# Optimization experiments

Measured on AMD Instinct MI355X. Metric: run time of the kernel, lower is better.

## Reference

```python
import jax, jax.numpy as jnp
import numpy as np

B, T, H, L, V = 32, 512, 1024, 256, 13  # V = FDIM_JOINT_VOCAB_DECODING


def setup_inputs() -> dict:
    key = jax.random.key(0)
    ks = jax.random.split(key, 16)
    s_in = 1.0 / np.sqrt(V)
    s_h = 1.0 / np.sqrt(H)
    s_l = 1.0 / np.sqrt(L)
    s_hl = 1.0 / np.sqrt(H + L)
    # one-hot-like teacher-forced inputs (first token is all-zero start token)
    labels = jax.random.randint(ks[0], (B, T), 0, V)
    seq_input = jax.nn.one_hot(labels, V, dtype=jnp.float32)
    seq_input = jnp.concatenate([jnp.zeros((B, 1, V), jnp.float32), seq_input[:, :-1]], axis=1)
    lengths = jax.random.randint(ks[1], (B,), T // 2, T + 1).astype(jnp.int32)
    return {
        "seq_input": seq_input,
        "latent_vec": jax.random.normal(ks[2], (B, L), jnp.float32),
        "labels": labels.astype(jnp.int32),
        "lengths": lengths,
        "W_ih": jax.random.uniform(ks[3], (4 * H, V), jnp.float32, -s_h, s_h),
        "W_hh": jax.random.uniform(ks[4], (4 * H, H), jnp.float32, -s_h, s_h),
        "b_ih": jax.random.uniform(ks[5], (4 * H,), jnp.float32, -s_h, s_h),
        "b_hh": jax.random.uniform(ks[6], (4 * H,), jnp.float32, -s_h, s_h),
        "Wz": jax.random.uniform(ks[7], (H, L), jnp.float32, -s_l, s_l),
        "bz": jax.random.uniform(ks[8], (H,), jnp.float32, -s_l, s_l),
        "Wnl": jax.random.uniform(ks[9], (H, H + L), jnp.float32, -s_hl, s_hl),
        "bnl": jax.random.uniform(ks[10], (H,), jnp.float32, -s_hl, s_hl),
        "Wout": jax.random.uniform(ks[11], (V, H), jnp.float32, -s_h, s_h),
        "bout": jax.random.uniform(ks[12], (V,), jnp.float32, -s_h, s_h),
    }


def _forward(seq_input, latent_vec, labels, lengths,
             W_ih, W_hh, b_ih, b_hh, Wz, bz, Wnl, bnl, Wout, bout):
    h0 = jax.nn.relu(latent_vec @ Wz.T + bz)              # [B,H]
    c0 = jnp.zeros_like(h0)

    def step(carry, x_t):
        h, c = carry
        gates = x_t @ W_ih.T + b_ih + h @ W_hh.T + b_hh   # [B,4H]
        i, f, g, o = jnp.split(gates, 4, axis=-1)         # torch LSTMCell gate order
        c = jax.nn.sigmoid(f) * c + jax.nn.sigmoid(i) * jnp.tanh(g)
        h = jax.nn.sigmoid(o) * jnp.tanh(c)
        return (h, c), h

    xs = jnp.swapaxes(seq_input, 0, 1)                    # [T,B,V]
    _, hs = jax.lax.scan(step, (h0, c0), xs)              # [T,B,H]
    hs = jnp.swapaxes(hs, 0, 1)                           # [B,T,H]

    # aggregate: cat(h, z) -> relu(W_nonlinear) -> W
    lat = jnp.broadcast_to(latent_vec[:, None, :], (hs.shape[0], hs.shape[1], latent_vec.shape[-1]))
    feat = jnp.concatenate([hs, lat], axis=-1)            # [B,T,H+L]
    logits = jax.nn.relu(feat @ Wnl.T + bnl) @ Wout.T + bout  # [B,T,V]

    logp = jax.nn.log_softmax(logits, axis=-1)
    nll = -jnp.take_along_axis(logp, labels[..., None].astype(jnp.int32), axis=-1)[..., 0]  # [B,T]
    mask = (jnp.arange(T)[None, :] < lengths[:, None]).astype(nll.dtype)
    batch_loss = jnp.sum(nll * mask, axis=1)              # per-sequence segment sum
    return batch_loss


def reference(seq_input, latent_vec, labels, lengths,
              W_ih, W_hh, b_ih, b_hh, Wz, bz, Wnl, bnl, Wout, bout):
    batch_loss = _forward(seq_input, latent_vec, labels, lengths,
                          W_ih, W_hh, b_ih, b_hh, Wz, bz, Wnl, bnl, Wout, bout)
    return jnp.sum(batch_loss), batch_loss
```

## Files before the change

### kernel.cpp

```cpp
#include <hip/hip_runtime.h>
#include <hip/hip_bf16.h>

#define B_   32
#define T_   512
#define H_   1024
#define L_   256
#define V_   13
#define G4H  4096
#define KHL  1280

typedef float f32x4 __attribute__((ext_vector_type(4)));
typedef short s16x8 __attribute__((ext_vector_type(8)));
typedef unsigned short u16;
typedef unsigned int   u32;
typedef unsigned long long u64;

#define OFF_BF   33619968u
#define OFF_BF2  42008576u
#define OFF_AZ   44630016u
#define OFF_BAR  44646400u
#define OFF_MID  44650496u
#define OFF_GX   OFF_MID
#define OFF_TOK  (OFF_MID + 229376u)

__device__ __forceinline__ u16 f2bf(float f) {
    union { float f; u32 u; } v; v.f = f;
    u32 u = v.u;
    u32 r = (u + 0x7fffu + ((u >> 16) & 1u)) >> 16;
    return (u16)r;
}
__device__ __forceinline__ float bf2f(u16 h) {
    union { u32 u; float f; } v; v.u = ((u32)h) << 16;
    return v.f;
}
__device__ __forceinline__ float sigm_(float x) {
    x = fminf(fmaxf(x, -30.f), 30.f);
    return 1.f / (1.f + __expf(-x));
}
__device__ __forceinline__ float tanh_(float x) {
    x = fminf(fmaxf(x, -15.f), 15.f);
    float e = __expf(2.f * x);
    return (e - 1.f) / (e + 1.f);
}

__device__ __forceinline__ u32 afrag_pos(int bl, int k) {
    return (u32)((k >> 5) * 512 + ((bl | (((k >> 3) & 3) << 4)) << 3) + (k & 7));
}

__global__ __launch_bounds__(256) void k_init_misc(
        const float* __restrict__ latent, const float* __restrict__ Wz,
        const float* __restrict__ bz,
        u16* __restrict__ Ax, u16* __restrict__ Az, int* __restrict__ bar) {
    int gid = blockIdx.x * 256 + threadIdx.x;
    int b = gid >> 10, j = gid & 1023;
    const float* lrow = latent + b * L_;
    const float* wrow = Wz + j * L_;
    float acc = bz[j];
    #pragma unroll 4
    for (int l = 0; l < L_; ++l) acc += lrow[l] * wrow[l];
    Ax[(b >> 4) * 16384 + afrag_pos(b & 15, j)] = f2bf(fmaxf(acc, 0.f));
    if (gid < B_ * L_) {
        int bb = gid >> 8, l = gid & 255;
        Az[(bb >> 4) * 4096 + afrag_pos(bb & 15, l)] = f2bf(latent[gid]);
    }
    if (gid < 1024) bar[gid] = 0;
}

__global__ __launch_bounds__(256) void k_init_gx(
        const float* __restrict__ W_ih, const float* __restrict__ b_ih,
        const float* __restrict__ b_hh, float* __restrict__ Gx) {
    int row = blockIdx.x * 256 + threadIdx.x;
    if (row >= G4H) return;
    int gg = row >> 10, jg = row & 1023;
    float base = b_ih[row] + b_hh[row];
    float* d = Gx + (size_t)jg * 56;
    const float* wr = W_ih + (size_t)row * V_;
    #pragma unroll
    for (int t = 0; t < V_; ++t) d[t * 4 + gg] = base + wr[t];
    d[13 * 4 + gg] = base;
}

__global__ __launch_bounds__(256) void k_init_tok(
        const float* __restrict__ seq, u16* __restrict__ tok) {
    int gid = blockIdx.x * 256 + threadIdx.x;
    int s = gid >> 5, b = gid & 31;
    const float* r = seq + ((size_t)b * T_ + s) * V_;
    int t = 13;
    #pragma unroll
    for (int v = 0; v < V_; ++v) if (r[v] > 0.5f) t = v;
    tok[gid] = (u16)t;
}

__global__ __launch_bounds__(256) void k_init_wfrag(
        const float* __restrict__ W_hh, u16* __restrict__ Bf) {
    int base = blockIdx.x * 256 + threadIdx.x;
    #pragma unroll
    for (int i = 0; i < 8; ++i) {
        int idx = base + i * 524288;
        int jv   = idx & 7;
        int lane = (idx >> 3) & 63;
        int kc   = (idx >> 9) & 31;
        int nt   = idx >> 14;
        int u = lane & 15;
        int row = (u & 3) * H_ + nt * 4 + (u >> 2);
        int k = kc * 32 + (lane >> 4) * 8 + jv;
        Bf[idx] = f2bf(W_hh[row * H_ + k]);
    }
}

__global__ __launch_bounds__(256) void k_init_wfrag2(
        const float* __restrict__ Wnl, u16* __restrict__ Bf2) {
    int idx = blockIdx.x * 256 + threadIdx.x;
    for (; idx < 1310720; idx += 524288) {
        int jv   = idx & 7;
        int lane = (idx >> 3) & 63;
        int q    = idx >> 9;
        int kc   = q % 40;
        int nt2  = q / 40;
        int n = nt2 * 16 + (lane & 15);
        int k = kc * 32 + (lane >> 4) * 8 + jv;
        Bf2[idx] = f2bf(Wnl[n * KHL + k]);
    }
}

__global__ __launch_bounds__(512, 1) void k_recur(
        const u16* __restrict__ tokbuf, const float* __restrict__ Gx,
        const u16* __restrict__ Bf, u16* __restrict__ Ax,
        int* __restrict__ bar) {
    __shared__ uint4 AhV[2048];
    __shared__ int sh_info;
    int tid = threadIdx.x;

    if (tid == 0) {
        u32 xcc = 0;
        asm volatile("s_getreg_b32 %0, hwreg(HW_REG_XCC_ID)" : "=s"(xcc));
        xcc &= 7u;
        int t = -1;
        if (xcc < 2u) {
            int tk = __hip_atomic_fetch_add(bar + (int)xcc * 512, 1,
                         __ATOMIC_RELAXED, __HIP_MEMORY_SCOPE_AGENT);
            if (tk < 32) t = ((int)xcc << 5) | tk;
        }
        sh_info = t;
    }
    __syncthreads();
    int info = sh_info;
    if (info < 0) return;
    int mt = info >> 5;
    int p  = info & 31;

    int w = tid >> 6, L = tid & 63;
    int nt = p * 8 + w;
    int lm = L & 15, quad = L >> 4;

    s16x8 afr[32];
    {
        const u16* bfp = Bf + (size_t)nt * 16384 + L * 8;
        #pragma unroll
        for (int kc = 0; kc < 32; ++kc)
            afr[kc] = *reinterpret_cast<const s16x8*>(bfp + kc * 512);
    }
    int jg = nt * 4 + quad;
    int b = mt * 16 + lm;
    const float* gxp = Gx + (size_t)jg * 56;
    u32 posu16 = (u32)((nt >> 3) * 512 + ((lm | (((nt >> 1) & 3) << 4)) << 3)
                       + (nt & 1) * 4 + quad);
    int* flags = bar + mt * 512 + 16;
    const int* myflag = flags + (w + 8 * (L & 3)) * 8;
    u32* AxD = (u32*)Ax;
    float c = 0.f;

    for (int s = 0; s < T_; ++s) {
        int tok = tokbuf[s * 32 + b];
        float4 gx4 = *reinterpret_cast<const float4*>(gxp + tok * 4);

        for (;;) {
            int v = __hip_atomic_load(myflag, __ATOMIC_RELAXED,
                                      __HIP_MEMORY_SCOPE_AGENT);
            if (__all(v >= s)) break;
            __builtin_amdgcn_s_sleep(1);
        }
        const uint4* srcq = (const uint4*)((const char*)Ax
                             + ((size_t)s * 2 + mt) * 32768);
        #pragma unroll
        for (int i = 0; i < 4; ++i)
            AhV[i * 512 + tid] = srcq[i * 512 + tid];
        __syncthreads();

        f32x4 a0 = {0.f,0.f,0.f,0.f}, a1 = {0.f,0.f,0.f,0.f};
        f32x4 a2 = {0.f,0.f,0.f,0.f}, a3 = {0.f,0.f,0.f,0.f};
        const u16* hp = (const u16*)AhV + L * 8;
        #pragma unroll
        for (int kc = 0; kc < 32; kc += 4) {
            s16x8 h0 = *reinterpret_cast<const s16x8*>(hp + kc * 512);
            s16x8 h1 = *reinterpret_cast<const s16x8*>(hp + (kc + 1) * 512);
            s16x8 h2 = *reinterpret_cast<const s16x8*>(hp + (kc + 2) * 512);
            s16x8 h3 = *reinterpret_cast<const s16x8*>(hp + (kc + 3) * 512);
            a0 = __builtin_amdgcn_mfma_f32_16x16x32_bf16(afr[kc],     h0, a0, 0, 0, 0);
            a1 = __builtin_amdgcn_mfma_f32_16x16x32_bf16(afr[kc + 1], h1, a1, 0, 0, 0);
            a2 = __builtin_amdgcn_mfma_f32_16x16x32_bf16(afr[kc + 2], h2, a2, 0, 0, 0);
            a3 = __builtin_amdgcn_mfma_f32_16x16x32_bf16(afr[kc + 3], h3, a3, 0, 0, 0);
        }
        float gi = a0[0] + a1[0] + a2[0] + a3[0] + gx4.x;
        float gf = a0[1] + a1[1] + a2[1] + a3[1] + gx4.y;
        float gg = a0[2] + a1[2] + a2[2] + a3[2] + gx4.z;
        float go = a0[3] + a1[3] + a2[3] + a3[3] + gx4.w;
        float ig = sigm_(gi), fg = sigm_(gf);
        float gt = tanh_(gg), og = sigm_(go);
        c = fg * c + ig * gt;
        float hv = og * tanh_(c);

        u32 bits = (u32)f2bf(hv);
        u32 other = (u32)(u16)__shfl_xor((int)bits, 16);
        if (!(quad & 1)) {
            u32 word = bits | (other << 16);
            AxD[((size_t)(s + 1) * 2 + mt) * 8192 + (posu16 >> 1)] = word;
        }
        if (s == T_ - 1) break;
        __syncthreads();
        if (tid == 0)
            __hip_atomic_store(flags + p * 8, s + 1, __ATOMIC_RELAXED,
                               __HIP_MEMORY_SCOPE_WORKGROUP);
    }
}

__global__ __launch_bounds__(256) void k_gemm1(
        const u16* __restrict__ Ax, const u16* __restrict__ Az,
        const u16* __restrict__ Bf2, const float* __restrict__ bnl,
        u16* __restrict__ mid) {
    int tid = threadIdx.x;
    int nb = blockIdx.x;
    int mb = blockIdx.y;
    int w = tid >> 6, L = tid & 63;
    int lm = L & 15, quad = L >> 4;
    int mti0 = mb * 8 + w * 2;
    const u16* a0p = Ax + ((size_t)mti0 + 2) * 16384 + L * 8;
    const u16* a1p = a0p + 16384;
    const u16* az0 = Az + L * 8;
    const u16* az1 = az0 + 4096;
    const u16* bp = Bf2 + (size_t)(nb * 4) * 40 * 512 + L * 8;

    f32x4 acc[2][4];
    #pragma unroll
    for (int a = 0; a < 2; ++a)
        #pragma unroll
        for (int n = 0; n < 4; ++n) acc[a][n] = (f32x4){0.f, 0.f, 0.f, 0.f};

    #pragma unroll 4
    for (int kc = 0; kc < 32; ++kc) {
        s16x8 a0 = *reinterpret_cast<const s16x8*>(a0p + kc * 512);
        s16x8 a1 = *reinterpret_cast<const s16x8*>(a1p + kc * 512);
        #pragma unroll
        for (int n4 = 0; n4 < 4; ++n4) {
            s16x8 bv = *reinterpret_cast<const s16x8*>(bp + ((size_t)n4 * 40 + kc) * 512);
            acc[0][n4] = __builtin_amdgcn_mfma_f32_16x16x32_bf16(a0, bv, acc[0][n4], 0, 0, 0);
            acc[1][n4] = __builtin_amdgcn_mfma_f32_16x16x32_bf16(a1, bv, acc[1][n4], 0, 0, 0);
        }
    }
    #pragma unroll
    for (int kc2 = 0; kc2 < 8; ++kc2) {
        s16x8 a0 = *reinterpret_cast<const s16x8*>(az0 + kc2 * 512);
        s16x8 a1 = *reinterpret_cast<const s16x8*>(az1 + kc2 * 512);
        #pragma unroll
        for (int n4 = 0; n4 < 4; ++n4) {
            s16x8 bv = *reinterpret_cast<const s16x8*>(bp + ((size_t)n4 * 40 + 32 + kc2) * 512);
            acc[0][n4] = __builtin_amdgcn_mfma_f32_16x16x32_bf16(a0, bv, acc[0][n4], 0, 0, 0);
            acc[1][n4] = __builtin_amdgcn_mfma_f32_16x16x32_bf16(a1, bv, acc[1][n4], 0, 0, 0);
        }
    }
    #pragma unroll
    for (int mt2 = 0; mt2 < 2; ++mt2)
        #pragma unroll
        for (int n4 = 0; n4 < 4; ++n4)
            #pragma unroll
            for (int r = 0; r < 4; ++r) {
                int m = mb * 128 + w * 32 + mt2 * 16 + quad * 4 + r;
                int n = (nb * 4 + n4) * 16 + lm;
                float v = acc[mt2][n4][r] + bnl[n];
                mid[(size_t)m * H_ + n] = f2bf(fmaxf(v, 0.f));
            }
}

__global__ __launch_bounds__(256) void k_loss(
        const u16* __restrict__ mid, const float* __restrict__ Wout,
        const float* __restrict__ bout, const int* __restrict__ labels,
        const int* __restrict__ lengths, float* __restrict__ out) {
    int mrow = blockIdx.x;
    int b = mrow & 31, t = mrow >> 5;
    if (t >= lengths[b]) return;
    int tid = threadIdx.x;
    float p[V_];
    #pragma unroll
    for (int v = 0; v < V_; ++v) p[v] = 0.f;
    uint2 raw = *reinterpret_cast<const uint2*>(mid + (size_t)mrow * H_ + tid * 4);
    const u16* rs = (const u16*)&raw;
    float mv0 = bf2f(rs[0]), mv1 = bf2f(rs[1]), mv2 = bf2f(rs[2]), mv3 = bf2f(rs[3]);
    #pragma unroll
    for (int v = 0; v < V_; ++v) {
        float4 wv = *reinterpret_cast<const float4*>(Wout + v * H_ + tid * 4);
        p[v] = mv0 * wv.x + mv1 * wv.y + mv2 * wv.z + mv3 * wv.w;
    }
    #pragma unroll
    for (int off = 32; off > 0; off >>= 1)
        #pragma unroll
        for (int v = 0; v < V_; ++v) p[v] += __shfl_down(p[v], off);
    __shared__ float red[4][V_];
    int w = tid >> 6, L = tid & 63;
    if (L == 0)
        #pragma unroll
        for (int v = 0; v < V_; ++v) red[w][v] = p[v];
    __syncthreads();
    if (tid == 0) {
        float lg[V_]; float mx = -1e30f;
        #pragma unroll
        for (int v = 0; v < V_; ++v) {
            lg[v] = red[0][v] + red[1][v] + red[2][v] + red[3][v] + bout[v];
            mx = fmaxf(mx, lg[v]);
        }
        float se = 0.f;
        #pragma unroll
        for (int v = 0; v < V_; ++v) se += __expf(lg[v] - mx);
        float lse = mx + logf(se);
        int lab = labels[b * T_ + t];
        atomicAdd(&out[1 + b], lse - lg[lab]);
    }
}

__global__ void k_final(float* __restrict__ out) {
    float s = 0.f;
    for (int b = 0; b < B_; ++b) s += out[1 + b];
    out[0] = s;
}

extern "C" void kernel_launch(void* const* d_in, const int* in_sizes, int n_in,
                              void* d_out, int out_size, void* d_ws, size_t ws_size,
                              hipStream_t stream) {
    const float* seq    = (const float*)d_in[0];
    const float* latent = (const float*)d_in[1];
    const int*   labels = (const int*)d_in[2];
    const int*   lengths= (const int*)d_in[3];
    const float* W_ih   = (const float*)d_in[4];
    const float* W_hh   = (const float*)d_in[5];
    const float* b_ih   = (const float*)d_in[6];
    const float* b_hh   = (const float*)d_in[7];
    const float* Wz     = (const float*)d_in[8];
    const float* bz     = (const float*)d_in[9];
    const float* Wnl    = (const float*)d_in[10];
    const float* bnl    = (const float*)d_in[11];
    const float* Wout   = (const float*)d_in[12];
    const float* bout   = (const float*)d_in[13];

    char* ws = (char*)d_ws;
    u16*   Ax   = (u16*)(ws);
    u16*   Bf   = (u16*)(ws + OFF_BF);
    u16*   Bf2  = (u16*)(ws + OFF_BF2);
    u16*   Az   = (u16*)(ws + OFF_AZ);
    int*   bar  = (int*)(ws + OFF_BAR);
    u16*   mid  = (u16*)(ws + OFF_MID);
    float* Gx   = (float*)(ws + OFF_GX);
    u16*   tok  = (u16*)(ws + OFF_TOK);
    float* out  = (float*)d_out;

    hipMemsetAsync(d_out, 0, 33 * sizeof(float), stream);
    k_init_misc<<<128, 256, 0, stream>>>(latent, Wz, bz, Ax, Az, bar);
    k_init_gx<<<16, 256, 0, stream>>>(W_ih, b_ih, b_hh, Gx);
    k_init_tok<<<64, 256, 0, stream>>>(seq, tok);
    k_init_wfrag<<<2048, 256, 0, stream>>>(W_hh, Bf);
    k_init_wfrag2<<<2048, 256, 0, stream>>>(Wnl, Bf2);
    k_recur<<<512, 512, 0, stream>>>(tok, Gx, Bf, Ax, bar);
    k_gemm1<<<dim3(16, 128), 256, 0, stream>>>(Ax, Az, Bf2, bnl, mid);
    k_loss<<<16384, 256, 0, stream>>>(mid, Wout, bout, labels, lengths, out);
    k_final<<<1, 1, 0, stream>>>(out);
}
```

Measured before the change: 1.194 ms.

## Split recurrent K dimension across waves with LDS reduction in LSTM step

Each wave now handles four gate tiles over one quarter of the hidden K range instead of one tile over the full K. The partial results are reduced through shared memory by the first wave group, which then applies the gate nonlinearities. This reuses each h fragment across four MFMAs and shortens each wave's serial MFMA chain per step. The cost is an extra barrier and LDS round trip every timestep, and only a quarter of the waves take part in the elementwise phase.

```diff
diff --git a/kernel.cpp b/kernel.cpp
--- a/kernel.cpp
+++ b/kernel.cpp
@@ -128,6 +128,7 @@
         const u16* __restrict__ Bf, u16* __restrict__ Ax,
         int* __restrict__ bar) {
     __shared__ uint4 AhV[2048];
+    __shared__ float redbuf[6][1088];
     __shared__ int sh_info;
     int tid = threadIdx.x;
 
@@ -150,29 +151,42 @@
     int p  = info & 31;
 
     int w = tid >> 6, L = tid & 63;
-    int nt = p * 8 + w;
+    int g = w & 1;
+    int q = w >> 1;
     int lm = L & 15, quad = L >> 4;
-
-    s16x8 afr[32];
-    {
-        const u16* bfp = Bf + (size_t)nt * 16384 + L * 8;
-        #pragma unroll
-        for (int kc = 0; kc < 32; ++kc)
-            afr[kc] = *reinterpret_cast<const s16x8*>(bfp + kc * 512);
-    }
-    int jg = nt * 4 + quad;
+    int nt0 = p * 8 + g * 4;
+
+    s16x8 afr[4][8];
+    #pragma unroll
+    for (int j = 0; j < 4; ++j) {
+        const u16* bfp = Bf + (size_t)(nt0 + j) * 16384 + (q * 8) * 512 + L * 8;
+        #pragma unroll
+        for (int kk = 0; kk < 8; ++kk)
+            afr[j][kk] = *reinterpret_cast<const s16x8*>(bfp + kk * 512);
+    }
     int b = mt * 16 + lm;
-    const float* gxp = Gx + (size_t)jg * 56;
-    u32 posu16 = (u32)((nt >> 3) * 512 + ((lm | (((nt >> 1) & 3) << 4)) << 3)
-                       + (nt & 1) * 4 + quad);
+    const float* gxp[4];
+    u32 pos[4];
+    #pragma unroll
+    for (int j = 0; j < 4; ++j) {
+        int ntj = nt0 + j;
+        gxp[j] = Gx + (size_t)(ntj * 4 + quad) * 56;
+        pos[j] = (u32)((ntj >> 3) * 512 + ((lm | (((ntj >> 1) & 3) << 4)) << 3)
+                       + (ntj & 1) * 4 + quad);
+    }
     int* flags = bar + mt * 512 + 16;
     const int* myflag = flags + (w + 8 * (L & 3)) * 8;
     u32* AxD = (u32*)Ax;
-    float c = 0.f;
+    float c0 = 0.f, c1 = 0.f, c2 = 0.f, c3 = 0.f;
 
     for (int s = 0; s < T_; ++s) {
         int tok = tokbuf[s * 32 + b];
-        float4 gx4 = *reinterpret_cast<const float4*>(gxp + tok * 4);
+        float4 gx4[4];
+        if (q == 0) {
+            #pragma unroll
+            for (int j = 0; j < 4; ++j)
+                gx4[j] = *reinterpret_cast<const float4*>(gxp[j] + tok * 4);
+        }
 
         for (;;) {
             int v = __hip_atomic_load(myflag, __ATOMIC_RELAXED,
@@ -187,34 +201,55 @@
             AhV[i * 512 + tid] = srcq[i * 512 + tid];
         __syncthreads();
 
-        f32x4 a0 = {0.f,0.f,0.f,0.f}, a1 = {0.f,0.f,0.f,0.f};
-        f32x4 a2 = {0.f,0.f,0.f,0.f}, a3 = {0.f,0.f,0.f,0.f};
-        const u16* hp = (const u16*)AhV + L * 8;
-        #pragma unroll
-        for (int kc = 0; kc < 32; kc += 4) {
-            s16x8 h0 = *reinterpret_cast<const s16x8*>(hp + kc * 512);
-            s16x8 h1 = *reinterpret_cast<const s16x8*>(hp + (kc + 1) * 512);
-            s16x8 h2 = *reinterpret_cast<const s16x8*>(hp + (kc + 2) * 512);
-            s16x8 h3 = *reinterpret_cast<const s16x8*>(hp + (kc + 3) * 512);
-            a0 = __builtin_amdgcn_mfma_f32_16x16x32_bf16(afr[kc],     h0, a0, 0, 0, 0);
-            a1 = __builtin_amdgcn_mfma_f32_16x16x32_bf16(afr[kc + 1], h1, a1, 0, 0, 0);
-            a2 = __builtin_amdgcn_mfma_f32_16x16x32_bf16(afr[kc + 2], h2, a2, 0, 0, 0);
-            a3 = __builtin_amdgcn_mfma_f32_16x16x32_bf16(afr[kc + 3], h3, a3, 0, 0, 0);
-        }
-        float gi = a0[0] + a1[0] + a2[0] + a3[0] + gx4.x;
-        float gf = a0[1] + a1[1] + a2[1] + a3[1] + gx4.y;
-        float gg = a0[2] + a1[2] + a2[2] + a3[2] + gx4.z;
-        float go = a0[3] + a1[3] + a2[3] + a3[3] + gx4.w;
-        float ig = sigm_(gi), fg = sigm_(gf);
-        float gt = tanh_(gg), og = sigm_(go);
-        c = fg * c + ig * gt;
-        float hv = og * tanh_(c);
-
-        u32 bits = (u32)f2bf(hv);
-        u32 other = (u32)(u16)__shfl_xor((int)bits, 16);
-        if (!(quad & 1)) {
-            u32 word = bits | (other << 16);
-            AxD[((size_t)(s + 1) * 2 + mt) * 8192 + (posu16 >> 1)] = word;
+        f32x4 acc[4];
+        #pragma unroll
+        for (int j = 0; j < 4; ++j) acc[j] = (f32x4){0.f, 0.f, 0.f, 0.f};
+        const u16* hp = (const u16*)AhV + (q * 8) * 512 + L * 8;
+        #pragma unroll
+        for (int kk = 0; kk < 8; ++kk) {
+            s16x8 h = *reinterpret_cast<const s16x8*>(hp + kk * 512);
+            acc[0] = __builtin_amdgcn_mfma_f32_16x16x32_bf16(afr[0][kk], h, acc[0], 0, 0, 0);
+            acc[1] = __builtin_amdgcn_mfma_f32_16x16x32_bf16(afr[1][kk], h, acc[1], 0, 0, 0);
+            acc[2] = __builtin_amdgcn_mfma_f32_16x16x32_bf16(afr[2][kk], h, acc[2], 0, 0, 0);
+            acc[3] = __builtin_amdgcn_mfma_f32_16x16x32_bf16(afr[3][kk], h, acc[3], 0, 0, 0);
+        }
+        if (q > 0) {
+            float* rb = &redbuf[(q - 1) * 2 + g][L * 17];
+            #pragma unroll
+            for (int j = 0; j < 4; ++j)
+                #pragma unroll
+                for (int r = 0; r < 4; ++r) rb[j * 4 + r] = acc[j][r];
+        }
+        __syncthreads();
+
+        if (q == 0) {
+            #pragma unroll
+            for (int qq = 0; qq < 3; ++qq) {
+                const float* rb = &redbuf[qq * 2 + g][L * 17];
+                #pragma unroll
+                for (int j = 0; j < 4; ++j)
+                    #pragma unroll
+                    for (int r = 0; r < 4; ++r) acc[j][r] += rb[j * 4 + r];
+            }
+            float* cs[4] = {&c0, &c1, &c2, &c3};
+            #pragma unroll
+            for (int j = 0; j < 4; ++j) {
+                float gi = acc[j][0] + gx4[j].x;
+                float gf = acc[j][1] + gx4[j].y;
+                float gg = acc[j][2] + gx4[j].z;
+                float go = acc[j][3] + gx4[j].w;
+                float ig = sigm_(gi), fg = sigm_(gf);
+                float gt = tanh_(gg), og = sigm_(go);
+                float cn = fg * (*cs[j]) + ig * gt;
+                *cs[j] = cn;
+                float hv = og * tanh_(cn);
+                u32 bits = (u32)f2bf(hv);
+                u32 other = (u32)(u16)__shfl_xor((int)bits, 16);
+                if (!(quad & 1)) {
+                    u32 word = bits | (other << 16);
+                    AxD[((size_t)(s + 1) * 2 + mt) * 8192 + (pos[j] >> 1)] = word;
+                }
+            }
         }
         if (s == T_ - 1) break;
         __syncthreads();
```

Result: slower. 1.578 ms (+32.2%).

## Halve recurrent workgroup size, each wave computes two gate tiles

Applied to the files above, without the earlier changes.

The persistent LSTM recurrence kernel now runs 4 waves per block instead of 8, and each wave holds W_hh fragments for two N-tiles (64 VGPR vectors) and reuses every LDS h fragment across both tiles. The h-state copy into LDS and the flag polling pattern are adjusted to match. The aim is to cut per-step LDS reads and barrier cost by sharing loaded h data across two MFMA chains. In exchange, register pressure doubles, which risks spills, and each wave does twice the serial MFMA work per step.

```diff
diff --git a/kernel.cpp b/kernel.cpp
--- a/kernel.cpp
+++ b/kernel.cpp
@@ -123,7 +123,7 @@
     }
 }
 
-__global__ __launch_bounds__(512, 1) void k_recur(
+__global__ __launch_bounds__(256, 1) void k_recur(
         const u16* __restrict__ tokbuf, const float* __restrict__ Gx,
         const u16* __restrict__ Bf, u16* __restrict__ Ax,
         int* __restrict__ bar) {
@@ -150,29 +150,36 @@
     int p  = info & 31;
 
     int w = tid >> 6, L = tid & 63;
-    int nt = p * 8 + w;
     int lm = L & 15, quad = L >> 4;
-
-    s16x8 afr[32];
-    {
-        const u16* bfp = Bf + (size_t)nt * 16384 + L * 8;
+    int nt0 = p * 8 + w * 2;
+
+    s16x8 afr[2][32];
+    #pragma unroll
+    for (int j = 0; j < 2; ++j) {
+        const u16* bfp = Bf + (size_t)(nt0 + j) * 16384 + L * 8;
         #pragma unroll
         for (int kc = 0; kc < 32; ++kc)
-            afr[kc] = *reinterpret_cast<const s16x8*>(bfp + kc * 512);
-    }
-    int jg = nt * 4 + quad;
+            afr[j][kc] = *reinterpret_cast<const s16x8*>(bfp + kc * 512);
+    }
     int b = mt * 16 + lm;
-    const float* gxp = Gx + (size_t)jg * 56;
-    u32 posu16 = (u32)((nt >> 3) * 512 + ((lm | (((nt >> 1) & 3) << 4)) << 3)
-                       + (nt & 1) * 4 + quad);
+    const float* gxp[2];
+    u32 pos[2];
+    #pragma unroll
+    for (int j = 0; j < 2; ++j) {
+        int ntj = nt0 + j;
+        gxp[j] = Gx + (size_t)(ntj * 4 + quad) * 56;
+        pos[j] = (u32)((ntj >> 3) * 512 + ((lm | (((ntj >> 1) & 3) << 4)) << 3)
+                       + (ntj & 1) * 4 + quad);
+    }
     int* flags = bar + mt * 512 + 16;
-    const int* myflag = flags + (w + 8 * (L & 3)) * 8;
+    const int* myflag = flags + (4 * (L & 7) + w) * 8;
     u32* AxD = (u32*)Ax;
-    float c = 0.f;
+    float c0 = 0.f, c1 = 0.f;
 
     for (int s = 0; s < T_; ++s) {
         int tok = tokbuf[s * 32 + b];
-        float4 gx4 = *reinterpret_cast<const float4*>(gxp + tok * 4);
+        float4 gx40 = *reinterpret_cast<const float4*>(gxp[0] + tok * 4);
+        float4 gx41 = *reinterpret_cast<const float4*>(gxp[1] + tok * 4);
 
         for (;;) {
             int v = __hip_atomic_load(myflag, __ATOMIC_RELAXED,
@@ -183,38 +190,50 @@
         const uint4* srcq = (const uint4*)((const char*)Ax
                              + ((size_t)s * 2 + mt) * 32768);
         #pragma unroll
-        for (int i = 0; i < 4; ++i)
-            AhV[i * 512 + tid] = srcq[i * 512 + tid];
+        for (int i = 0; i < 8; ++i)
+            AhV[i * 256 + tid] = srcq[i * 256 + tid];
         __syncthreads();
 
-        f32x4 a0 = {0.f,0.f,0.f,0.f}, a1 = {0.f,0.f,0.f,0.f};
-        f32x4 a2 = {0.f,0.f,0.f,0.f}, a3 = {0.f,0.f,0.f,0.f};
+        f32x4 a00 = {0.f,0.f,0.f,0.f}, a01 = {0.f,0.f,0.f,0.f};
+        f32x4 a10 = {0.f,0.f,0.f,0.f}, a11 = {0.f,0.f,0.f,0.f};
         const u16* hp = (const u16*)AhV + L * 8;
         #pragma unroll
-        for (int kc = 0; kc < 32; kc += 4) {
-            s16x8 h0 = *reinterpret_cast<const s16x8*>(hp + kc * 512);
-            s16x8 h1 = *reinterpret_cast<const s16x8*>(hp + (kc + 1) * 512);
-            s16x8 h2 = *reinterpret_cast<const s16x8*>(hp + (kc + 2) * 512);
-            s16x8 h3 = *reinterpret_cast<const s16x8*>(hp + (kc + 3) * 512);
-            a0 = __builtin_amdgcn_mfma_f32_16x16x32_bf16(afr[kc],     h0, a0, 0, 0, 0);
-            a1 = __builtin_amdgcn_mfma_f32_16x16x32_bf16(afr[kc + 1], h1, a1, 0, 0, 0);
-            a2 = __builtin_amdgcn_mfma_f32_16x16x32_bf16(afr[kc + 2], h2, a2, 0, 0, 0);
-            a3 = __builtin_amdgcn_mfma_f32_16x16x32_bf16(afr[kc + 3], h3, a3, 0, 0, 0);
-        }
-        float gi = a0[0] + a1[0] + a2[0] + a3[0] + gx4.x;
-        float gf = a0[1] + a1[1] + a2[1] + a3[1] + gx4.y;
-        float gg = a0[2] + a1[2] + a2[2] + a3[2] + gx4.z;
-        float go = a0[3] + a1[3] + a2[3] + a3[3] + gx4.w;
-        float ig = sigm_(gi), fg = sigm_(gf);
-        float gt = tanh_(gg), og = sigm_(go);
-        c = fg * c + ig * gt;
-        float hv = og * tanh_(c);
-
-        u32 bits = (u32)f2bf(hv);
-        u32 other = (u32)(u16)__shfl_xor((int)bits, 16);
-        if (!(quad & 1)) {
-            u32 word = bits | (other << 16);
-            AxD[((size_t)(s + 1) * 2 + mt) * 8192 + (posu16 >> 1)] = word;
+        for (int kc = 0; kc < 16; kc += 2) {
+            s16x8 ha0 = *reinterpret_cast<const s16x8*>(hp + kc * 512);
+            s16x8 hb0 = *reinterpret_cast<const s16x8*>(hp + (kc + 16) * 512);
+            s16x8 ha1 = *reinterpret_cast<const s16x8*>(hp + (kc + 1) * 512);
+            s16x8 hb1 = *reinterpret_cast<const s16x8*>(hp + (kc + 17) * 512);
+            a00 = __builtin_amdgcn_mfma_f32_16x16x32_bf16(afr[0][kc],      ha0, a00, 0, 0, 0);
+            a10 = __builtin_amdgcn_mfma_f32_16x16x32_bf16(afr[1][kc],      ha0, a10, 0, 0, 0);
+            a01 = __builtin_amdgcn_mfma_f32_16x16x32_bf16(afr[0][kc + 16], hb0, a01, 0, 0, 0);
+            a11 = __builtin_amdgcn_mfma_f32_16x16x32_bf16(afr[1][kc + 16], hb0, a11, 0, 0, 0);
+            a00 = __builtin_amdgcn_mfma_f32_16x16x32_bf16(afr[0][kc + 1],  ha1, a00, 0, 0, 0);
+            a10 = __builtin_amdgcn_mfma_f32_16x16x32_bf16(afr[1][kc + 1],  ha1, a10, 0, 0, 0);
+            a01 = __builtin_amdgcn_mfma_f32_16x16x32_bf16(afr[0][kc + 17], hb1, a01, 0, 0, 0);
+            a11 = __builtin_amdgcn_mfma_f32_16x16x32_bf16(afr[1][kc + 17], hb1, a11, 0, 0, 0);
+        }
+
+        #pragma unroll
+        for (int j = 0; j < 2; ++j) {
+            f32x4 aa = (j == 0) ? a00 : a10;
+            f32x4 ab = (j == 0) ? a01 : a11;
+            float4 gx4 = (j == 0) ? gx40 : gx41;
+            float gi = aa[0] + ab[0] + gx4.x;
+            float gf = aa[1] + ab[1] + gx4.y;
+            float gg = aa[2] + ab[2] + gx4.z;
+            float go = aa[3] + ab[3] + gx4.w;
+            float ig = sigm_(gi), fg = sigm_(gf);
+            float gt = tanh_(gg), og = sigm_(go);
+            float cc = (j == 0) ? c0 : c1;
+            cc = fg * cc + ig * gt;
+            if (j == 0) c0 = cc; else c1 = cc;
+            float hv = og * tanh_(cc);
+            u32 bits = (u32)f2bf(hv);
+            u32 other = (u32)(u16)__shfl_xor((int)bits, 16);
+            if (!(quad & 1)) {
+                u32 word = bits | (other << 16);
+                AxD[((size_t)(s + 1) * 2 + mt) * 8192 + (pos[j] >> 1)] = word;
+            }
         }
         if (s == T_ - 1) break;
         __syncthreads();
@@ -367,7 +386,7 @@
     k_init_tok<<<64, 256, 0, stream>>>(seq, tok);
     k_init_wfrag<<<2048, 256, 0, stream>>>(W_hh, Bf);
     k_init_wfrag2<<<2048, 256, 0, stream>>>(Wnl, Bf2);
-    k_recur<<<512, 512, 0, stream>>>(tok, Gx, Bf, Ax, bar);
+    k_recur<<<512, 256, 0, stream>>>(tok, Gx, Bf, Ax, bar);
     k_gemm1<<<dim3(16, 128), 256, 0, stream>>>(Ax, Az, Bf2, bnl, mid);
     k_loss<<<16384, 256, 0, stream>>>(mid, Wout, bout, labels, lengths, out);
     k_final<<<1, 1, 0, stream>>>(out);
```

Result: slower. 2.258 ms (+89.1%).
